# Performance work log

Hardware: AMD Instinct MI355X
Metric: run time of the kernel (lower is better)

Reference implementation:

```python
import jax, jax.numpy as jnp
import numpy as np
from jax import lax


def setup_inputs() -> dict:
    key = jax.random.key(0)
    ks = jax.random.split(key, 6)
    num_u, num_v, num_h, batch = 64, 256, 256, 8192
    # lecun_normal: std = 1/sqrt(fan_in) where fan_in is the last dim
    def lecun(k, shape):
        return jax.random.normal(k, shape, dtype=jnp.float32) * jnp.sqrt(1.0 / shape[1])
    return {
        "u_state": (jax.random.uniform(ks[0], (batch, num_u)) < 0.5).astype(jnp.float32),
        "weights_vu": lecun(ks[1], (num_v, num_u)),
        "weights_hu": lecun(ks[2], (num_h, num_u)),
        "weights_hv": lecun(ks[3], (num_h, num_v)),
        "bias_v": jax.random.normal(ks[4], (num_v,), dtype=jnp.float32) * 0.01,
        "bias_h": jax.random.normal(ks[5], (num_h,), dtype=jnp.float32) * 0.01,
        "therm_steps": 24,
        "size": 8,
    }


def reference(u_state, weights_vu, weights_hu, weights_hv, bias_v, bias_h,
              therm_steps, size):
    """ConditionalRBM.sample: init visible from u, thermalize therm_steps
    Gibbs sweeps, then collect `size` consecutive Gibbs samples."""
    key = jax.random.key(1)

    def bern(k, p):
        # binomial(n=1, p) == bernoulli(p)
        return (jax.random.uniform(k, p.shape) < p).astype(jnp.float32)

    def gibbs_step(v, k):
        k1, k2 = jax.random.split(k)
        ph = jax.nn.sigmoid(v @ weights_hv.T + u_state @ weights_hu.T + bias_h)  # [B,H]
        h = bern(k1, ph)
        pv = jax.nn.sigmoid(h @ weights_hv + u_state @ weights_vu.T + bias_v)    # [B,V]
        return bern(k2, pv)

    ks = jax.random.split(key, therm_steps + size + 1)
    # initial visible state from the conditional prior p(v|u)
    v0 = bern(ks[0], jax.nn.sigmoid(u_state @ weights_vu.T + bias_v))
    # thermalization chain (sequential, loop-carried)
    v_therm, _ = lax.scan(lambda v, k: (gibbs_step(v, k), None), v0, ks[1:1 + therm_steps])
    # sampling chain, stack the `size` samples
    def sample_step(v, k):
        v_new = gibbs_step(v, k)
        return v_new, v_new
    _, samples = lax.scan(sample_step, v_therm, ks[1 + therm_steps:])
    return samples.astype(jnp.uint8)  # [size, B, V]
```

## Files before the change

kernel.cpp:

```cpp
#include <hip/hip_runtime.h>
#include <cstdint>
#include <cstddef>


#pragma clang fp contract(off)

#define BATCH 8192
#define NU 64
#define NF 256
#define RPB 16
#define TPB 512
#define CH 16
#define NCH (NF / CH)
#define RTI 16
#define THERM 24
#define NSAMP 8
#define NSTEP (THERM + NSAMP)

__host__ __device__ __forceinline__ void tf2x32(uint32_t k0, uint32_t k1,
                                                uint32_t x0, uint32_t x1,
                                                uint32_t* o0, uint32_t* o1) {
  uint32_t ks2 = k0 ^ k1 ^ 0x1BD11BDAu;
  x0 += k0; x1 += k1;
#define TFR(r) { x0 += x1; x1 = (x1 << (r)) | (x1 >> (32 - (r))); x1 ^= x0; }
  TFR(13) TFR(15) TFR(26) TFR(6)
  x0 += k1;  x1 += ks2 + 1u;
  TFR(17) TFR(29) TFR(16) TFR(24)
  x0 += ks2; x1 += k0 + 2u;
  TFR(13) TFR(15) TFR(26) TFR(6)
  x0 += k0;  x1 += k1 + 3u;
  TFR(17) TFR(29) TFR(16) TFR(24)
  x0 += k1;  x1 += ks2 + 4u;
  TFR(13) TFR(15) TFR(26) TFR(6)
  x0 += ks2; x1 += k0 + 5u;
#undef TFR
  *o0 = x0; *o1 = x1;
}

__device__ __forceinline__ float xla_expf(float x) {
  float xc = fminf(x, 88.3762626647950f);
  xc = fmaxf(xc, -88.3762626647949f);
  float fx = floorf(__builtin_fmaf(xc, 1.44269504088896341f, 0.5f));
  float tmp = 0.693359375f * fx;
  float z = -2.12194440e-4f * fx;
  float r = xc - tmp;
  r = r - z;
  z = r * r;
  float y = __builtin_fmaf(r, 1.9875691500e-4f, 1.3981999507e-3f);
  y = __builtin_fmaf(y, r, 8.3334519073e-3f);
  y = __builtin_fmaf(y, r, 4.1665795894e-2f);
  y = __builtin_fmaf(y, r, 1.6666665459e-1f);
  y = __builtin_fmaf(y, r, 5.0000001201e-1f);
  y = __builtin_fmaf(y, z, r);
  y = y + 1.0f;
  int n = (int)fx;
  float p2 = __int_as_float((n + 127) << 23);
  float res = y * p2;
  return fmaxf(res, x);
}

__device__ __forceinline__ float sigmoid_ref(float x) {
  float e = xla_expf(-x);
  return 1.0f / (1.0f + e);
}

__device__ __forceinline__ float bern_sample(uint32_t key0, uint32_t key1,
                                             uint32_t idx, float p) {
  uint32_t b0, b1;
  tf2x32(key0, key1, 0u, idx, &b0, &b1);
  uint32_t bits = b0 ^ b1;
  float u = __uint_as_float((bits >> 9) | 0x3f800000u) - 1.0f;
  return (u < p) ? 1.0f : 0.0f;
}

__device__ __forceinline__ void gld_lds16(const float* g, float* l) {
  __builtin_amdgcn_global_load_lds(
      (const __attribute__((address_space(1))) void*)g,
      (__attribute__((address_space(3))) void*)l, 16, 0, 0);
}

__global__ void k_transpose(const float* __restrict__ Whv,
                            float* __restrict__ WhvT) {
  int j = threadIdx.x;
  int k = blockIdx.x;
  WhvT[k * NF + j] = Whv[j * NF + k];
}

__global__ __launch_bounds__(256, 2) void k_udot(const float* __restrict__ U,
                                                 const float* __restrict__ W,
                                                 float* __restrict__ out) {
  __shared__ __align__(16) float Ulds[NU * RTI];
  const int j = threadIdx.x;
  const int i0 = blockIdx.x * RTI;
  const int si = j & 15;
  const int sg = j >> 4;
  {
    float4 u4 = *(const float4*)(U + (size_t)(i0 + si) * NU + sg * 4);
    Ulds[(sg * 4 + 0) * RTI + si] = u4.x;
    Ulds[(sg * 4 + 1) * RTI + si] = u4.y;
    Ulds[(sg * 4 + 2) * RTI + si] = u4.z;
    Ulds[(sg * 4 + 3) * RTI + si] = u4.w;
  }
  float wreg[NU];
  const float4* wr4 = (const float4*)(W + (size_t)j * NU);
#pragma unroll
  for (int r = 0; r < NU / 4; ++r) {
    float4 t = wr4[r];
    wreg[4 * r + 0] = t.x; wreg[4 * r + 1] = t.y;
    wreg[4 * r + 2] = t.z; wreg[4 * r + 3] = t.w;
  }
  __syncthreads();
  float acc[RTI];
#pragma unroll
  for (int i = 0; i < RTI; ++i) acc[i] = 0.0f;
#pragma unroll
  for (int kk = 0; kk < NU; ++kk) {
    const float w = wreg[kk];
    const float4 s0 = *(const float4*)(&Ulds[kk * RTI + 0]);
    const float4 s1 = *(const float4*)(&Ulds[kk * RTI + 4]);
    const float4 s2 = *(const float4*)(&Ulds[kk * RTI + 8]);
    const float4 s3 = *(const float4*)(&Ulds[kk * RTI + 12]);
    acc[0]  = __builtin_fmaf(s0.x, w, acc[0]);
    acc[1]  = __builtin_fmaf(s0.y, w, acc[1]);
    acc[2]  = __builtin_fmaf(s0.z, w, acc[2]);
    acc[3]  = __builtin_fmaf(s0.w, w, acc[3]);
    acc[4]  = __builtin_fmaf(s1.x, w, acc[4]);
    acc[5]  = __builtin_fmaf(s1.y, w, acc[5]);
    acc[6]  = __builtin_fmaf(s1.z, w, acc[6]);
    acc[7]  = __builtin_fmaf(s1.w, w, acc[7]);
    acc[8]  = __builtin_fmaf(s2.x, w, acc[8]);
    acc[9]  = __builtin_fmaf(s2.y, w, acc[9]);
    acc[10] = __builtin_fmaf(s2.z, w, acc[10]);
    acc[11] = __builtin_fmaf(s2.w, w, acc[11]);
    acc[12] = __builtin_fmaf(s3.x, w, acc[12]);
    acc[13] = __builtin_fmaf(s3.y, w, acc[13]);
    acc[14] = __builtin_fmaf(s3.z, w, acc[14]);
    acc[15] = __builtin_fmaf(s3.w, w, acc[15]);
  }
#pragma unroll
  for (int i = 0; i < RTI; ++i)
    out[(size_t)(i0 + i) * NF + j] = acc[i];
}

__global__ __launch_bounds__(TPB, 4) void k_chain(
    const float* __restrict__ Whv, const float* __restrict__ WhvT,
    const float* __restrict__ uh, const float* __restrict__ uv,
    const float* __restrict__ bh, const float* __restrict__ bv,
    int* __restrict__ out) {
  __shared__ __align__(16) float Wbuf[2][CH * NF];
  __shared__ uint32_t bitsL[2][RPB * 8];
  __shared__ uint32_t nib[RPB * 64];
  __shared__ float biasL[2][NF];
  __shared__ uint32_t ksL[66];
  __shared__ uint32_t keysL[NSTEP * 4];

  const int t = threadIdx.x;
  const int rowbase = blockIdx.x * RPB;
  const int rg = t >> 6;
  const int cgg = t & 63;
  const int jc = cgg * 4;

  float4 cuh[2], cuv[2];
#pragma unroll
  for (int ri = 0; ri < 2; ++ri) {
    const int lr = rg * 2 + ri;
    cuh[ri] = *(const float4*)(uh + (size_t)(rowbase + lr) * NF + jc);
    cuv[ri] = *(const float4*)(uv + (size_t)(rowbase + lr) * NF + jc);
  }

  if (t < NF) {
    biasL[0][t] = bh[t];
    biasL[1][t] = bv[t];
  }
  if (t < 33) tf2x32(0u, 1u, 0u, (uint32_t)t, &ksL[2 * t], &ksL[2 * t + 1]);
  __syncthreads();
  if (t < NSTEP) {
    uint32_t a = ksL[2 * (1 + t)], b2 = ksL[2 * (1 + t) + 1];
    tf2x32(a, b2, 0u, 0u, &keysL[4 * t + 0], &keysL[4 * t + 1]);
    tf2x32(a, b2, 0u, 1u, &keysL[4 * t + 2], &keysL[4 * t + 3]);
  }
  __syncthreads();

  {
    const uint32_t k0 = ksL[0], k1 = ksL[1];
#pragma unroll
    for (int ri = 0; ri < 2; ++ri) {
      const int lr = rg * 2 + ri;
      const int row = rowbase + lr;
      const float4 b4 = *(const float4*)(&biasL[1][jc]);
      const uint32_t idx0 = (uint32_t)(row * NF + jc);
      uint32_t nb = 0;
      nb |= (bern_sample(k0, k1, idx0 + 0,
                 sigmoid_ref(cuv[ri].x + b4.x)) != 0.0f ? 1u : 0u);
      nb |= (bern_sample(k0, k1, idx0 + 1,
                 sigmoid_ref(cuv[ri].y + b4.y)) != 0.0f ? 2u : 0u);
      nb |= (bern_sample(k0, k1, idx0 + 2,
                 sigmoid_ref(cuv[ri].z + b4.z)) != 0.0f ? 4u : 0u);
      nb |= (bern_sample(k0, k1, idx0 + 3,
                 sigmoid_ref(cuv[ri].w + b4.w)) != 0.0f ? 8u : 0u);
      nib[lr * 64 + cgg] = nb;
    }
  }
  __syncthreads();
  if (t < 128) {
    const int lr = t >> 3, wo = t & 7;
    const uint32_t* nn = &nib[lr * 64 + wo * 8];
    uint32_t wrd = 0;
#pragma unroll
    for (int g = 0; g < 8; ++g) wrd |= nn[g] << (4 * g);
    bitsL[0][lr * 8 + wo] = wrd;
  }
  __syncthreads();

#pragma unroll 1
  for (int tt = 0; tt < NSTEP; ++tt) {
#pragma unroll 1
    for (int ph = 0; ph < 2; ++ph) {
      const float* M = ph ? Whv : WhvT;
      const uint32_t* sb = bitsL[ph];
      uint32_t* db = bitsL[ph ^ 1];
      const float* bl = biasL[ph];
      const uint32_t k0 = keysL[4 * tt + 2 * ph + 0];
      const uint32_t k1 = keysL[4 * tt + 2 * ph + 1];
      int* smp = (ph == 1 && tt >= THERM)
                     ? out + (size_t)(tt - THERM) * BATCH * NF
                     : (int*)nullptr;

      float acc[8];
#pragma unroll
      for (int q = 0; q < 8; ++q) acc[q] = 0.0f;

#pragma unroll
      for (int q = 0; q < 2; ++q)
        gld_lds16(M + (size_t)(q * TPB + t) * 4, &Wbuf[0][(q * TPB + t) * 4]);
      __syncthreads();

#pragma unroll 1
      for (int c = 0; c < NCH; ++c) {
        if (c + 1 < NCH) {
          const float* src = M + (size_t)(c + 1) * CH * NF;
          float* dst = Wbuf[(c + 1) & 1];
#pragma unroll
          for (int q = 0; q < 2; ++q)
            gld_lds16(src + (size_t)(q * TPB + t) * 4,
                      &dst[(q * TPB + t) * 4]);
        }
        const int wi = c >> 1;
        const int hs = (c & 1) * 16;
        const uint32_t wd0 =
            __builtin_amdgcn_readfirstlane(sb[(rg * 2 + 0) * 8 + wi]) >> hs;
        const uint32_t wd1 =
            __builtin_amdgcn_readfirstlane(sb[(rg * 2 + 1) * 8 + wi]) >> hs;
        const float* wl = &Wbuf[c & 1][jc];
#pragma unroll
        for (int kk = 0; kk < CH; ++kk) {
          const float4 w = *(const float4*)(wl + kk * NF);
          const float s0 = (wd0 & (1u << kk)) ? 1.0f : 0.0f;
          const float s1 = (wd1 & (1u << kk)) ? 1.0f : 0.0f;
          acc[0] = __builtin_fmaf(s0, w.x, acc[0]);
          acc[1] = __builtin_fmaf(s0, w.y, acc[1]);
          acc[2] = __builtin_fmaf(s0, w.z, acc[2]);
          acc[3] = __builtin_fmaf(s0, w.w, acc[3]);
          acc[4] = __builtin_fmaf(s1, w.x, acc[4]);
          acc[5] = __builtin_fmaf(s1, w.y, acc[5]);
          acc[6] = __builtin_fmaf(s1, w.z, acc[6]);
          acc[7] = __builtin_fmaf(s1, w.w, acc[7]);
        }
        __syncthreads();
      }

      const float4 b4 = *(const float4*)(bl + jc);
#pragma unroll
      for (int ri = 0; ri < 2; ++ri) {
        const int lr = rg * 2 + ri;
        const int row = rowbase + lr;
        const float4 c4 = ph ? cuv[ri] : cuh[ri];
        const uint32_t idx0 = (uint32_t)(row * NF + jc);
        const float v0 = bern_sample(k0, k1, idx0 + 0,
            sigmoid_ref((acc[ri * 4 + 0] + c4.x) + b4.x));
        const float v1 = bern_sample(k0, k1, idx0 + 1,
            sigmoid_ref((acc[ri * 4 + 1] + c4.y) + b4.y));
        const float v2 = bern_sample(k0, k1, idx0 + 2,
            sigmoid_ref((acc[ri * 4 + 2] + c4.z) + b4.z));
        const float v3 = bern_sample(k0, k1, idx0 + 3,
            sigmoid_ref((acc[ri * 4 + 3] + c4.w) + b4.w));
        nib[lr * 64 + cgg] = (v0 != 0.0f ? 1u : 0u) |
                             (v1 != 0.0f ? 2u : 0u) |
                             (v2 != 0.0f ? 4u : 0u) |
                             (v3 != 0.0f ? 8u : 0u);
        if (smp) {
          int4 o;
          o.x = (v0 != 0.0f) ? 1 : 0;
          o.y = (v1 != 0.0f) ? 1 : 0;
          o.z = (v2 != 0.0f) ? 1 : 0;
          o.w = (v3 != 0.0f) ? 1 : 0;
          *(int4*)(smp + (size_t)row * NF + jc) = o;
        }
      }
      __syncthreads();
      if (t < 128) {
        const int lr = t >> 3, wo = t & 7;
        const uint32_t* nn = &nib[lr * 64 + wo * 8];
        uint32_t wrd = 0;
#pragma unroll
        for (int g = 0; g < 8; ++g) wrd |= nn[g] << (4 * g);
        db[lr * 8 + wo] = wrd;
      }
      __syncthreads();
    }
  }
}

extern "C" void kernel_launch(void* const* d_in, const int* in_sizes, int n_in,
                              void* d_out, int out_size, void* d_ws, size_t ws_size,
                              hipStream_t stream) {
  const float* u_state = (const float*)d_in[0];
  const float* Wvu     = (const float*)d_in[1];
  const float* Whu     = (const float*)d_in[2];
  const float* Whv     = (const float*)d_in[3];
  const float* bv      = (const float*)d_in[4];
  const float* bh      = (const float*)d_in[5];
  int* out = (int*)d_out;

  float* ws   = (float*)d_ws;
  float* WhvT = ws;
  float* uh   = WhvT + NF * NF;
  float* uv   = uh + (size_t)BATCH * NF;

  k_transpose<<<NF, NF, 0, stream>>>(Whv, WhvT);
  k_udot<<<BATCH / RTI, NF, 0, stream>>>(u_state, Whu, uh);
  k_udot<<<BATCH / RTI, NF, 0, stream>>>(u_state, Wvu, uv);
  k_chain<<<BATCH / RPB, TPB, 0, stream>>>(Whv, WhvT, uh, uv, bh, bv, out);

  (void)in_sizes; (void)n_in; (void)out_size; (void)ws_size;
}
```

Baseline: 1.503 ms.

## Retile chain kernel to four rows by two columns per thread with 32-row chunks

Changes the per-thread register tile in the Gibbs chain kernel from 2 rows x 4 columns to 4 rows x 2 columns, so each thread reads float2 weights from LDS instead of float4. Each weight value loaded is now reused across four batch rows, halving LDS read bytes per FMA. Weight chunks grow from 16 to 32 rows, which halves the number of chunk iterations and barriers but doubles the LDS staging buffer (64KB for the double buffer). The larger LDS footprint may cut how many blocks fit per CU.

```diff
diff --git a/kernel.cpp b/kernel.cpp
--- a/kernel.cpp
+++ b/kernel.cpp
@@ -10,7 +10,7 @@
 #define NF 256
 #define RPB 16
 #define TPB 512
-#define CH 16
+#define CH 32
 #define NCH (NF / CH)
 #define RTI 16
 #define THERM 24
@@ -149,23 +149,23 @@
     int* __restrict__ out) {
   __shared__ __align__(16) float Wbuf[2][CH * NF];
   __shared__ uint32_t bitsL[2][RPB * 8];
-  __shared__ uint32_t nib[RPB * 64];
+  __shared__ uint32_t nib[RPB * 128];
   __shared__ float biasL[2][NF];
   __shared__ uint32_t ksL[66];
   __shared__ uint32_t keysL[NSTEP * 4];
 
   const int t = threadIdx.x;
   const int rowbase = blockIdx.x * RPB;
-  const int rg = t >> 6;
-  const int cgg = t & 63;
-  const int jc = cgg * 4;
-
-  float4 cuh[2], cuv[2];
-#pragma unroll
-  for (int ri = 0; ri < 2; ++ri) {
-    const int lr = rg * 2 + ri;
-    cuh[ri] = *(const float4*)(uh + (size_t)(rowbase + lr) * NF + jc);
-    cuv[ri] = *(const float4*)(uv + (size_t)(rowbase + lr) * NF + jc);
+  const int rg = t >> 7;
+  const int cgg = t & 127;
+  const int jc = cgg * 2;
+
+  float2 cuh[4], cuv[4];
+#pragma unroll
+  for (int ri = 0; ri < 4; ++ri) {
+    const int lr = rg * 4 + ri;
+    cuh[ri] = *(const float2*)(uh + (size_t)(rowbase + lr) * NF + jc);
+    cuv[ri] = *(const float2*)(uv + (size_t)(rowbase + lr) * NF + jc);
   }
 
   if (t < NF) {
@@ -183,31 +183,27 @@
 
   {
     const uint32_t k0 = ksL[0], k1 = ksL[1];
-#pragma unroll
-    for (int ri = 0; ri < 2; ++ri) {
-      const int lr = rg * 2 + ri;
+    const float2 b2 = *(const float2*)(&biasL[1][jc]);
+#pragma unroll
+    for (int ri = 0; ri < 4; ++ri) {
+      const int lr = rg * 4 + ri;
       const int row = rowbase + lr;
-      const float4 b4 = *(const float4*)(&biasL[1][jc]);
       const uint32_t idx0 = (uint32_t)(row * NF + jc);
       uint32_t nb = 0;
       nb |= (bern_sample(k0, k1, idx0 + 0,
-                 sigmoid_ref(cuv[ri].x + b4.x)) != 0.0f ? 1u : 0u);
+                 sigmoid_ref(cuv[ri].x + b2.x)) != 0.0f ? 1u : 0u);
       nb |= (bern_sample(k0, k1, idx0 + 1,
-                 sigmoid_ref(cuv[ri].y + b4.y)) != 0.0f ? 2u : 0u);
-      nb |= (bern_sample(k0, k1, idx0 + 2,
-                 sigmoid_ref(cuv[ri].z + b4.z)) != 0.0f ? 4u : 0u);
-      nb |= (bern_sample(k0, k1, idx0 + 3,
-                 sigmoid_ref(cuv[ri].w + b4.w)) != 0.0f ? 8u : 0u);
-      nib[lr * 64 + cgg] = nb;
+                 sigmoid_ref(cuv[ri].y + b2.y)) != 0.0f ? 2u : 0u);
+      nib[lr * 128 + cgg] = nb;
     }
   }
   __syncthreads();
   if (t < 128) {
     const int lr = t >> 3, wo = t & 7;
-    const uint32_t* nn = &nib[lr * 64 + wo * 8];
+    const uint32_t* nn = &nib[lr * 128 + wo * 16];
     uint32_t wrd = 0;
 #pragma unroll
-    for (int g = 0; g < 8; ++g) wrd |= nn[g] << (4 * g);
+    for (int g = 0; g < 16; ++g) wrd |= nn[g] << (2 * g);
     bitsL[0][lr * 8 + wo] = wrd;
   }
   __syncthreads();
@@ -231,7 +227,7 @@
       for (int q = 0; q < 8; ++q) acc[q] = 0.0f;
 
 #pragma unroll
-      for (int q = 0; q < 2; ++q)
+      for (int q = 0; q < 4; ++q)
         gld_lds16(M + (size_t)(q * TPB + t) * 4, &Wbuf[0][(q * TPB + t) * 4]);
       __syncthreads();
 
@@ -241,69 +237,65 @@
           const float* src = M + (size_t)(c + 1) * CH * NF;
           float* dst = Wbuf[(c + 1) & 1];
 #pragma unroll
-          for (int q = 0; q < 2; ++q)
+          for (int q = 0; q < 4; ++q)
             gld_lds16(src + (size_t)(q * TPB + t) * 4,
                       &dst[(q * TPB + t) * 4]);
         }
-        const int wi = c >> 1;
-        const int hs = (c & 1) * 16;
         const uint32_t wd0 =
-            __builtin_amdgcn_readfirstlane(sb[(rg * 2 + 0) * 8 + wi]) >> hs;
+            __builtin_amdgcn_readfirstlane(sb[(rg * 4 + 0) * 8 + c]);
         const uint32_t wd1 =
-            __builtin_amdgcn_readfirstlane(sb[(rg * 2 + 1) * 8 + wi]) >> hs;
+            __builtin_amdgcn_readfirstlane(sb[(rg * 4 + 1) * 8 + c]);
+        const uint32_t wd2 =
+            __builtin_amdgcn_readfirstlane(sb[(rg * 4 + 2) * 8 + c]);
+        const uint32_t wd3 =
+            __builtin_amdgcn_readfirstlane(sb[(rg * 4 + 3) * 8 + c]);
         const float* wl = &Wbuf[c & 1][jc];
 #pragma unroll
         for (int kk = 0; kk < CH; ++kk) {
-          const float4 w = *(const float4*)(wl + kk * NF);
+          const float2 w = *(const float2*)(wl + kk * NF);
           const float s0 = (wd0 & (1u << kk)) ? 1.0f : 0.0f;
           const float s1 = (wd1 & (1u << kk)) ? 1.0f : 0.0f;
+          const float s2 = (wd2 & (1u << kk)) ? 1.0f : 0.0f;
+          const float s3 = (wd3 & (1u << kk)) ? 1.0f : 0.0f;
           acc[0] = __builtin_fmaf(s0, w.x, acc[0]);
           acc[1] = __builtin_fmaf(s0, w.y, acc[1]);
-          acc[2] = __builtin_fmaf(s0, w.z, acc[2]);
-          acc[3] = __builtin_fmaf(s0, w.w, acc[3]);
-          acc[4] = __builtin_fmaf(s1, w.x, acc[4]);
-          acc[5] = __builtin_fmaf(s1, w.y, acc[5]);
-          acc[6] = __builtin_fmaf(s1, w.z, acc[6]);
-          acc[7] = __builtin_fmaf(s1, w.w, acc[7]);
+          acc[2] = __builtin_fmaf(s1, w.x, acc[2]);
+          acc[3] = __builtin_fmaf(s1, w.y, acc[3]);
+          acc[4] = __builtin_fmaf(s2, w.x, acc[4]);
+          acc[5] = __builtin_fmaf(s2, w.y, acc[5]);
+          acc[6] = __builtin_fmaf(s3, w.x, acc[6]);
+          acc[7] = __builtin_fmaf(s3, w.y, acc[7]);
         }
         __syncthreads();
       }
 
-      const float4 b4 = *(const float4*)(bl + jc);
-#pragma unroll
-      for (int ri = 0; ri < 2; ++ri) {
-        const int lr = rg * 2 + ri;
+      const float2 b2 = *(const float2*)(bl + jc);
+#pragma unroll
+      for (int ri = 0; ri < 4; ++ri) {
+        const int lr = rg * 4 + ri;
         const int row = rowbase + lr;
-        const float4 c4 = ph ? cuv[ri] : cuh[ri];
+        const float2 c2 = ph ? cuv[ri] : cuh[ri];
         const uint32_t idx0 = (uint32_t)(row * NF + jc);
         const float v0 = bern_sample(k0, k1, idx0 + 0,
-            sigmoid_ref((acc[ri * 4 + 0] + c4.x) + b4.x));
+            sigmoid_ref((acc[ri * 2 + 0] + c2.x) + b2.x));
         const float v1 = bern_sample(k0, k1, idx0 + 1,
-            sigmoid_ref((acc[ri * 4 + 1] + c4.y) + b4.y));
-        const float v2 = bern_sample(k0, k1, idx0 + 2,
-            sigmoid_ref((acc[ri * 4 + 2] + c4.z) + b4.z));
-        const float v3 = bern_sample(k0, k1, idx0 + 3,
-            sigmoid_ref((acc[ri * 4 + 3] + c4.w) + b4.w));
-        nib[lr * 64 + cgg] = (v0 != 0.0f ? 1u : 0u) |
-                             (v1 != 0.0f ? 2u : 0u) |
-                             (v2 != 0.0f ? 4u : 0u) |
-                             (v3 != 0.0f ? 8u : 0u);
+            sigmoid_ref((acc[ri * 2 + 1] + c2.y) + b2.y));
+        nib[lr * 128 + cgg] = (v0 != 0.0f ? 1u : 0u) |
+                              (v1 != 0.0f ? 2u : 0u);
         if (smp) {
-          int4 o;
+          int2 o;
           o.x = (v0 != 0.0f) ? 1 : 0;
           o.y = (v1 != 0.0f) ? 1 : 0;
-          o.z = (v2 != 0.0f) ? 1 : 0;
-          o.w = (v3 != 0.0f) ? 1 : 0;
-          *(int4*)(smp + (size_t)row * NF + jc) = o;
+          *(int2*)(smp + (size_t)row * NF + jc) = o;
         }
       }
       __syncthreads();
       if (t < 128) {
         const int lr = t >> 3, wo = t & 7;
-        const uint32_t* nn = &nib[lr * 64 + wo * 8];
+        const uint32_t* nn = &nib[lr * 128 + wo * 16];
         uint32_t wrd = 0;
 #pragma unroll
-        for (int g = 0; g < 8; ++g) wrd |= nn[g] << (4 * g);
+        for (int g = 0; g < 16; ++g) wrd |= nn[g] << (2 * g);
         db[lr * 8 + wo] = wrd;
       }
       __syncthreads();
```

Result: slower. 1.762 ms (+17.2%).
